# Optimization experiments

Measured on AMD Instinct MI355X. Metric: run time of the kernel, lower is better.

## Reference

```python
import jax, jax.numpy as jnp
import numpy as np

N_NODES = 100000
N_EDGES = 1600000
F_IN = 128
HID = 64
N_LAYERS = 4
N_GRAPHS = 512
N_CLASSES = 10
BN_EPS = 1e-5


def setup_inputs() -> dict:
    key = jax.random.key(0)
    ks = jax.random.split(key, 24)
    inp = {
        "x": jax.random.normal(ks[0], (N_NODES, F_IN), dtype=jnp.float32),
        "edge_index": jax.random.randint(ks[1], (2, N_EDGES), 0, N_NODES, dtype=jnp.int32),
        "batch": jnp.sort(jax.random.randint(ks[2], (N_NODES,), 0, N_GRAPHS, dtype=jnp.int32)),
        # GINConv eps (train_eps=True, init 0) per layer
        "eps": jnp.zeros((N_LAYERS,), dtype=jnp.float32),
        # layer 0 MLP (in=F_IN)
        "W1_0": jax.random.normal(ks[3], (F_IN, HID)) * 0.05,
        "b1_0": jnp.zeros((HID,)),
        "g_0": jnp.ones((HID,)),
        "be_0": jnp.zeros((HID,)),
        "W2_0": jax.random.normal(ks[4], (HID, HID)) * 0.05,
        "b2_0": jnp.zeros((HID,)),
        # layers 1..3 MLPs stacked (in=HID)
        "W1_r": jax.random.normal(ks[5], (N_LAYERS - 1, HID, HID)) * 0.05,
        "b1_r": jnp.zeros((N_LAYERS - 1, HID)),
        "g_r": jnp.ones((N_LAYERS - 1, HID)),
        "be_r": jnp.zeros((N_LAYERS - 1, HID)),
        "W2_r": jax.random.normal(ks[6], (N_LAYERS - 1, HID, HID)) * 0.05,
        "b2_r": jnp.zeros((N_LAYERS - 1, HID)),
        # head
        "lin1_W": jax.random.normal(ks[7], (N_LAYERS * HID, HID)) * 0.05,
        "lin1_b": jnp.zeros((HID,)),
        "bn_g": jnp.ones((HID,)),
        "bn_b": jnp.zeros((HID,)),
        "lin2_W": jax.random.normal(ks[8], (HID, N_CLASSES)) * 0.05,
        "lin2_b": jnp.zeros((N_CLASSES,)),
    }
    return inp


def _bn(h, g, b):
    # BatchNorm1d training-mode math: biased variance over the batch dim
    mu = h.mean(axis=0)
    var = h.var(axis=0)
    return (h - mu) * jax.lax.rsqrt(var + BN_EPS) * g + b


def _gin_conv(x, src, dst, eps, W1, b1, g, be, W2, b2):
    # sum of neighbor (source) features scattered to target nodes
    agg = jax.ops.segment_sum(x[src], dst, num_segments=N_NODES)
    h = (1.0 + eps) * x + agg
    h = jax.nn.relu(_bn(h @ W1 + b1, g, be))
    h = jax.nn.relu(h @ W2 + b2)
    return h


def reference(x, edge_index, batch, eps,
              W1_0, b1_0, g_0, be_0, W2_0, b2_0,
              W1_r, b1_r, g_r, be_r, W2_r, b2_r,
              lin1_W, lin1_b, bn_g, bn_b, lin2_W, lin2_b):
    src, dst = edge_index[0], edge_index[1]
    h = _gin_conv(x, src, dst, eps[0], W1_0, b1_0, g_0, be_0, W2_0, b2_0)
    xs = [h]
    for i in range(N_LAYERS - 1):
        h = _gin_conv(h, src, dst, eps[i + 1], W1_r[i], b1_r[i], g_r[i], be_r[i], W2_r[i], b2_r[i])
        xs.append(h)
    hcat = jnp.concatenate(xs, axis=-1)                      # [N, L*HID]
    pooled = jax.ops.segment_sum(hcat, batch, num_segments=N_GRAPHS)  # [G, L*HID]
    out = pooled @ lin1_W + lin1_b
    out = jax.nn.relu(_bn(out, bn_g, bn_b))
    # dropout: eval mode (identity)
    out = out @ lin2_W + lin2_b
    return jax.nn.log_softmax(out, axis=-1)
```

## Files before the change

### kernel.cpp

```cpp
#include <hip/hip_runtime.h>

#define N_NODES 100000
#define N_EDGES 1600000
#define F_IN 128
#define HID 64
#define NLAYERS 4
#define N_GRAPHS 512
#define N_CLASSES 10

#define NB_BUCKET 256
#define NODES_PER_BUCKET 391
#define NBLK 256
#define EDGES_PER_BLK (N_EDGES / NBLK)

#define N_TILES ((N_NODES + 63) / 64)
#define FUSED_GRID 1024
#define NAGG 2048
#define NSTAT 512

typedef unsigned int uint_t;
typedef unsigned short ushort_t;

__device__ __forceinline__ float lo_bf(uint_t w) { return __uint_as_float(w << 16); }
__device__ __forceinline__ float hi_bf(uint_t w) { return __uint_as_float(w & 0xffff0000u); }
__device__ __forceinline__ ushort_t f2bf(float f) {
    uint_t u = __float_as_uint(f);
    u += 0x7fffu + ((u >> 16) & 1u);
    return (ushort_t)(u >> 16);
}
__device__ __forceinline__ uint_t pack2(float a, float b) {
    return ((uint_t)f2bf(b) << 16) | (uint_t)f2bf(a);
}

__global__ __launch_bounds__(256) void k_zero(int* __restrict__ btotal,
                                              float* __restrict__ statsA,
                                              float* __restrict__ pooled) {
    int i = blockIdx.x * 256 + threadIdx.x;
    if (i < NB_BUCKET) btotal[i] = 0;
    if (i < NLAYERS * 128) statsA[i] = 0.f;
    if (i < N_GRAPHS * 256) pooled[i] = 0.f;
}

__global__ __launch_bounds__(512) void kb_hist(const int* __restrict__ dst,
                                               int* __restrict__ partial,
                                               int* __restrict__ btotal) {
    __shared__ int h[NB_BUCKET];
    int tid = threadIdx.x;
    if (tid < NB_BUCKET) h[tid] = 0;
    __syncthreads();
    int e0 = blockIdx.x * EDGES_PER_BLK;
    for (int i = tid; i < EDGES_PER_BLK; i += 512) {
        uint_t d = (uint_t)dst[e0 + i];
        if (d >= (uint_t)N_NODES) d = N_NODES - 1;
        atomicAdd(&h[d / NODES_PER_BUCKET], 1);
    }
    __syncthreads();
    if (tid < NB_BUCKET) {
        int c = h[tid];
        partial[blockIdx.x * NB_BUCKET + tid] = c;
        if (c) atomicAdd(&btotal[tid], c);
    }
}

__global__ __launch_bounds__(256) void kb_base(const int* __restrict__ btotal,
                                               int* __restrict__ bbase) {
    __shared__ int sh[NB_BUCKET];
    int tid = threadIdx.x;
    sh[tid] = btotal[tid];
    __syncthreads();
    for (int off = 1; off < NB_BUCKET; off <<= 1) {
        int t = (tid >= off) ? sh[tid - off] : 0;
        __syncthreads();
        sh[tid] += t;
        __syncthreads();
    }
    bbase[tid + 1] = sh[tid];
    if (tid == 0) bbase[0] = 0;
}

__global__ __launch_bounds__(256) void kb_scan(const int* __restrict__ partial,
                                               const int* __restrict__ bbase,
                                               int* __restrict__ goff) {
    __shared__ int sh[NBLK];
    int b = blockIdx.x, tid = threadIdx.x;
    sh[tid] = partial[tid * NB_BUCKET + b];
    __syncthreads();
    for (int off = 1; off < NBLK; off <<= 1) {
        int t = (tid >= off) ? sh[tid - off] : 0;
        __syncthreads();
        sh[tid] += t;
        __syncthreads();
    }
    int excl = (tid == 0) ? 0 : sh[tid - 1];
    goff[tid * NB_BUCKET + b] = bbase[b] + excl;
}

__global__ __launch_bounds__(512) void kb_scatter(const int* __restrict__ src,
                                                  const int* __restrict__ dst,
                                                  const int* __restrict__ goff,
                                                  int* __restrict__ ebuf) {
    __shared__ int cur[NB_BUCKET];
    int tid = threadIdx.x;
    if (tid < NB_BUCKET) cur[tid] = goff[blockIdx.x * NB_BUCKET + tid];
    __syncthreads();
    int e0 = blockIdx.x * EDGES_PER_BLK;
    for (int i = tid; i < EDGES_PER_BLK; i += 512) {
        uint_t d = (uint_t)dst[e0 + i];
        if (d >= (uint_t)N_NODES) d = N_NODES - 1;
        uint_t s = (uint_t)src[e0 + i];
        if (s >= (uint_t)N_NODES) s = 0;
        int b = (int)(d / NODES_PER_BUCKET);
        int dl = (int)d - b * NODES_PER_BUCKET;
        int pos = atomicAdd(&cur[b], 1);
        ebuf[pos] = (dl << 17) | (int)s;
    }
}

__global__ __launch_bounds__(512) void kb_csr(const int* __restrict__ ebuf,
                                              const int* __restrict__ bbase,
                                              int* __restrict__ row_ptr,
                                              int* __restrict__ col_src) {
    __shared__ int cnt[512];
    __shared__ int sh[512];
    __shared__ int off[512];
    int tid = threadIdx.x, b = blockIdx.x;
    int s0 = bbase[b], s1 = bbase[b + 1];
    int n = s1 - s0;
    cnt[tid] = 0;
    __syncthreads();
    for (int i = tid; i < n; i += 512) {
        int dl = ebuf[s0 + i] >> 17;
        atomicAdd(&cnt[dl], 1);
    }
    __syncthreads();
    sh[tid] = cnt[tid];
    __syncthreads();
    for (int o = 1; o < 512; o <<= 1) {
        int t = (tid >= o) ? sh[tid - o] : 0;
        __syncthreads();
        sh[tid] += t;
        __syncthreads();
    }
    off[tid] = (tid == 0) ? 0 : sh[tid - 1];
    cnt[tid] = 0;

    int node0 = b * NODES_PER_BUCKET;
    int ncnt = N_NODES - node0;
    if (ncnt > NODES_PER_BUCKET) ncnt = NODES_PER_BUCKET;
    if (tid < ncnt) row_ptr[node0 + tid] = s0 + off[tid];
    if (b == NB_BUCKET - 1 && tid == 0) row_ptr[N_NODES] = N_EDGES;
    __syncthreads();

    for (int i = tid; i < n; i += 512) {
        int v = ebuf[s0 + i];
        int dl = v >> 17;
        int r = atomicAdd(&cnt[dl], 1);
        col_src[s0 + off[dl] + r] = v & 0x1FFFF;
    }
}

__global__ __launch_bounds__(256) void k_aggregate_u(const uint2* __restrict__ y2,
                                                     const int* __restrict__ row_ptr,
                                                     const int* __restrict__ col_src,
                                                     const float* __restrict__ eps, int layer,
                                                     const float* __restrict__ b1,
                                                     uint2* __restrict__ u2) {
    int wid = threadIdx.x >> 6, lane = threadIdx.x & 63;
    int gid = lane >> 4, l4 = lane & 15;
    float one_eps = 1.0f + eps[layer];
    int stride = gridDim.x * 4;

    for (int node = blockIdx.x * 4 + wid; node < N_NODES; node += stride) {
        int e0 = row_ptr[node], e1 = row_ptr[node + 1];
        if (e0 < 0) e0 = 0;
        if (e1 > N_EDGES) e1 = N_EDGES;
        if (e1 < e0) e1 = e0;

        float4 a0 = {0.f, 0.f, 0.f, 0.f}, a1 = a0, a2 = a0, a3 = a0;

        for (int ebase = e0; ebase < e1; ebase += 64) {
            int len = e1 - ebase; if (len > 64) len = 64;
            int ci = ebase + lane; if (ci > e1 - 1) ci = e1 - 1;
            int sv = col_src[ci];
            sv = (int)min((uint_t)sv, (uint_t)(N_NODES - 1));

            int nfull = len >> 2;
            int rem = len & 3;
            int j = 0;
            for (; j + 4 <= nfull; j += 4) {
                int s0 = __shfl(sv, (j + 0) * 4 + gid, 64);
                int s1 = __shfl(sv, (j + 1) * 4 + gid, 64);
                int s2 = __shfl(sv, (j + 2) * 4 + gid, 64);
                int s3 = __shfl(sv, (j + 3) * 4 + gid, 64);
                uint2 w0 = y2[(size_t)s0 * 16 + l4];
                uint2 w1 = y2[(size_t)s1 * 16 + l4];
                uint2 w2 = y2[(size_t)s2 * 16 + l4];
                uint2 w3 = y2[(size_t)s3 * 16 + l4];
                a0.x += lo_bf(w0.x); a0.y += hi_bf(w0.x); a0.z += lo_bf(w0.y); a0.w += hi_bf(w0.y);
                a1.x += lo_bf(w1.x); a1.y += hi_bf(w1.x); a1.z += lo_bf(w1.y); a1.w += hi_bf(w1.y);
                a2.x += lo_bf(w2.x); a2.y += hi_bf(w2.x); a2.z += lo_bf(w2.y); a2.w += hi_bf(w2.y);
                a3.x += lo_bf(w3.x); a3.y += hi_bf(w3.x); a3.z += lo_bf(w3.y); a3.w += hi_bf(w3.y);
            }
            for (; j < nfull; ++j) {
                int s = __shfl(sv, j * 4 + gid, 64);
                uint2 w = y2[(size_t)s * 16 + l4];
                a0.x += lo_bf(w.x); a0.y += hi_bf(w.x); a0.z += lo_bf(w.y); a0.w += hi_bf(w.y);
            }
            if (rem) {
                int s = __shfl(sv, nfull * 4 + gid, 64);
                if (gid < rem) {
                    uint2 w = y2[(size_t)s * 16 + l4];
                    a1.x += lo_bf(w.x); a1.y += hi_bf(w.x); a1.z += lo_bf(w.y); a1.w += hi_bf(w.y);
                }
            }
        }

        float4 t;
        t.x = (a0.x + a1.x) + (a2.x + a3.x);
        t.y = (a0.y + a1.y) + (a2.y + a3.y);
        t.z = (a0.z + a1.z) + (a2.z + a3.z);
        t.w = (a0.w + a1.w) + (a2.w + a3.w);
        t.x += __shfl_xor(t.x, 16, 64); t.x += __shfl_xor(t.x, 32, 64);
        t.y += __shfl_xor(t.y, 16, 64); t.y += __shfl_xor(t.y, 32, 64);
        t.z += __shfl_xor(t.z, 16, 64); t.z += __shfl_xor(t.z, 32, 64);
        t.w += __shfl_xor(t.w, 16, 64); t.w += __shfl_xor(t.w, 32, 64);

        if (gid == 0) {
            uint2 ws = y2[(size_t)node * 16 + l4];
            float4 bb = *(const float4*)&b1[4 * l4];
            float ox = t.x + one_eps * lo_bf(ws.x) + bb.x;
            float oy = t.y + one_eps * hi_bf(ws.x) + bb.y;
            float oz = t.z + one_eps * lo_bf(ws.y) + bb.z;
            float ow = t.w + one_eps * hi_bf(ws.y) + bb.w;
            uint2 o2;
            o2.x = pack2(ox, oy);
            o2.y = pack2(oz, ow);
            u2[(size_t)node * 16 + l4] = o2;
        }
    }
}

__global__ __launch_bounds__(256) void k_stats(const uint2* __restrict__ u2,
                                               float* __restrict__ partials) {
    __shared__ float sh[256 * 8];
    int tid = threadIdx.x;
    float a[4] = {0.f, 0.f, 0.f, 0.f}, b[4] = {0.f, 0.f, 0.f, 0.f};
    for (size_t i = (size_t)blockIdx.x * 256 + tid; i < (size_t)N_NODES * 16; i += (size_t)gridDim.x * 256) {
        uint2 w = u2[i];
        float v0 = lo_bf(w.x), v1 = hi_bf(w.x), v2 = lo_bf(w.y), v3 = hi_bf(w.y);
        a[0] += v0; b[0] += v0 * v0;
        a[1] += v1; b[1] += v1 * v1;
        a[2] += v2; b[2] += v2 * v2;
        a[3] += v3; b[3] += v3 * v3;
    }
    #pragma unroll
    for (int j = 0; j < 4; ++j) { sh[tid * 8 + j] = a[j]; sh[tid * 8 + 4 + j] = b[j]; }
    __syncthreads();
    if (tid < 64) {
        int quad = tid >> 2, o = tid & 3;
        float s = 0.f, ss = 0.f;
        for (int g = 0; g < 16; ++g) {
            int t = g * 16 + quad;
            s  += sh[t * 8 + o];
            ss += sh[t * 8 + 4 + o];
        }
        partials[(size_t)blockIdx.x * 128 + tid]      = s;
        partials[(size_t)blockIdx.x * 128 + 64 + tid] = ss;
    }
}

__global__ __launch_bounds__(256) void k_redstats(const float* __restrict__ partials,
                                                  float* __restrict__ outp) {
    __shared__ float sh[256];
    int b = blockIdx.x, tid = threadIdx.x;
    float v = 0.f;
    for (int i = tid; i < NSTAT; i += 256) v += partials[(size_t)i * 128 + b];
    sh[tid] = v;
    __syncthreads();
    for (int off = 128; off > 0; off >>= 1) {
        if (tid < off) sh[tid] += sh[tid + off];
        __syncthreads();
    }
    if (tid == 0) outp[b] = sh[0];
}

template <int K>
__global__ __launch_bounds__(256) void k_gemm1(const float* __restrict__ A,
                                               const float* __restrict__ W,
                                               ushort_t* __restrict__ out) {
    constexpr int KC = 64;
    constexpr int KP = KC + 4;
    __shared__ float Al[64 * KP];
    __shared__ float Wl[KC * 64];
    int tid = threadIdx.x;
    int base = blockIdx.x * 64;
    int ct = (tid & 15) * 4;
    int rb = (tid >> 4) * 4;
    float4 acc0 = {0.f, 0.f, 0.f, 0.f}, acc1 = acc0, acc2 = acc0, acc3 = acc0;
    bool full = (base + 64 <= N_NODES);

    #pragma unroll
    for (int kc = 0; kc < K; kc += KC) {
        for (int i = tid; i < KC * 16; i += 256)
            ((float4*)Wl)[i] = ((const float4*)(W + (size_t)kc * 64))[i];
        for (int i = tid; i < 64 * (KC / 4); i += 256) {
            int row = i / (KC / 4), kq = i % (KC / 4);
            int grow = base + row;
            if (!full && grow >= N_NODES) grow = N_NODES - 1;
            float4 v = ((const float4*)(A + (size_t)grow * K + kc))[kq];
            *(float4*)&Al[row * KP + kq * 4] = v;
        }
        __syncthreads();

        const float* A0 = &Al[(rb + 0) * KP];
        const float* A1 = &Al[(rb + 1) * KP];
        const float* A2 = &Al[(rb + 2) * KP];
        const float* A3 = &Al[(rb + 3) * KP];
        #pragma unroll 4
        for (int k = 0; k < KC; ++k) {
            float4 w = *(const float4*)&Wl[k * 64 + ct];
            float a0 = A0[k], a1 = A1[k], a2 = A2[k], a3 = A3[k];
            acc0.x = fmaf(a0, w.x, acc0.x); acc0.y = fmaf(a0, w.y, acc0.y);
            acc0.z = fmaf(a0, w.z, acc0.z); acc0.w = fmaf(a0, w.w, acc0.w);
            acc1.x = fmaf(a1, w.x, acc1.x); acc1.y = fmaf(a1, w.y, acc1.y);
            acc1.z = fmaf(a1, w.z, acc1.z); acc1.w = fmaf(a1, w.w, acc1.w);
            acc2.x = fmaf(a2, w.x, acc2.x); acc2.y = fmaf(a2, w.y, acc2.y);
            acc2.z = fmaf(a2, w.z, acc2.z); acc2.w = fmaf(a2, w.w, acc2.w);
            acc3.x = fmaf(a3, w.x, acc3.x); acc3.y = fmaf(a3, w.y, acc3.y);
            acc3.z = fmaf(a3, w.z, acc3.z); acc3.w = fmaf(a3, w.w, acc3.w);
        }
        __syncthreads();
    }

    float4 accs[4] = {acc0, acc1, acc2, acc3};
    #pragma unroll
    for (int r = 0; r < 4; ++r) {
        int row = base + rb + r;
        if (row < N_NODES) {
            ushort4 o;
            o.x = f2bf(accs[r].x); o.y = f2bf(accs[r].y);
            o.z = f2bf(accs[r].z); o.w = f2bf(accs[r].w);
            *(ushort4*)&out[(size_t)row * 64 + ct] = o;
        }
    }
}

template <bool NEXT>
__global__ __launch_bounds__(256) void k_fused(const uint2* __restrict__ U2,
                                               const float* __restrict__ W2,
                                               const float* __restrict__ sums,
                                               const float* __restrict__ g_,
                                               const float* __restrict__ be,
                                               const float* __restrict__ b2,
                                               const int* __restrict__ batch,
                                               float* __restrict__ pooled, int layer,
                                               const float* __restrict__ W1n,
                                               ushort_t* __restrict__ ynext) {
    constexpr int K = 64, KP = 68;
    __shared__ float Al[64 * KP];
    __shared__ float Wl[K * 64];
    __shared__ float Pl[256];
    __shared__ __align__(16) float Sc[64];
    __shared__ __align__(16) float Sh[64];
    int tid = threadIdx.x;

    if (tid < 64) {
        const float inv_n = 1.0f / N_NODES;
        float mean = sums[tid] * inv_n;
        float var = sums[64 + tid] * inv_n - mean * mean;
        if (var < 0.f) var = 0.f;
        float inv = rsqrtf(var + 1e-5f);
        float sc = inv * g_[tid];
        Sc[tid] = sc;
        Sh[tid] = be[tid] - mean * sc;
    }
    __syncthreads();

    int ct = (tid & 15) * 4;
    int rb = (tid >> 4) * 4;
    int r0 = tid >> 4, q0 = tid & 15;
    float4 scv = *(const float4*)&Sc[q0 * 4];
    float4 shv = *(const float4*)&Sh[q0 * 4];

    uint2 up0, up1, up2, up3;

    {
        int base = blockIdx.x * 64;
        int g0 = base + r0, g1 = base + r0 + 16, g2 = base + r0 + 32, g3 = base + r0 + 48;
        if (g0 > N_NODES - 1) g0 = N_NODES - 1;
        if (g1 > N_NODES - 1) g1 = N_NODES - 1;
        if (g2 > N_NODES - 1) g2 = N_NODES - 1;
        if (g3 > N_NODES - 1) g3 = N_NODES - 1;
        up0 = U2[(size_t)g0 * 16 + q0];
        up1 = U2[(size_t)g1 * 16 + q0];
        up2 = U2[(size_t)g2 * 16 + q0];
        up3 = U2[(size_t)g3 * 16 + q0];
    }

    for (int tile = blockIdx.x; tile < N_TILES; tile += gridDim.x) {
        int base = tile * 64;

        for (int i = tid; i < K * 16; i += 256)
            ((float4*)Wl)[i] = ((const float4*)W2)[i];
        {
            #define UNPK(UR, RR) { \
                float4 v = {lo_bf((UR).x), hi_bf((UR).x), lo_bf((UR).y), hi_bf((UR).y)}; \
                v.x = fmaxf(fmaf(v.x, scv.x, shv.x), 0.f); \
                v.y = fmaxf(fmaf(v.y, scv.y, shv.y), 0.f); \
                v.z = fmaxf(fmaf(v.z, scv.z, shv.z), 0.f); \
                v.w = fmaxf(fmaf(v.w, scv.w, shv.w), 0.f); \
                *(float4*)&Al[(RR) * KP + q0 * 4] = v; }
            UNPK(up0, r0);
            UNPK(up1, r0 + 16);
            UNPK(up2, r0 + 32);
            UNPK(up3, r0 + 48);
            #undef UNPK
        }
        __syncthreads();

        float4 acc0 = {0.f, 0.f, 0.f, 0.f}, acc1 = acc0, acc2 = acc0, acc3 = acc0;
        {
            const float* A0 = &Al[(rb + 0) * KP];
            const float* A1 = &Al[(rb + 1) * KP];
            const float* A2 = &Al[(rb + 2) * KP];
            const float* A3 = &Al[(rb + 3) * KP];
            #pragma unroll 4
            for (int k = 0; k < K; ++k) {
                float4 w = *(const float4*)&Wl[k * 64 + ct];
                float a0 = A0[k], a1 = A1[k], a2 = A2[k], a3 = A3[k];
                acc0.x = fmaf(a0, w.x, acc0.x); acc0.y = fmaf(a0, w.y, acc0.y);
                acc0.z = fmaf(a0, w.z, acc0.z); acc0.w = fmaf(a0, w.w, acc0.w);
                acc1.x = fmaf(a1, w.x, acc1.x); acc1.y = fmaf(a1, w.y, acc1.y);
                acc1.z = fmaf(a1, w.z, acc1.z); acc1.w = fmaf(a1, w.w, acc1.w);
                acc2.x = fmaf(a2, w.x, acc2.x); acc2.y = fmaf(a2, w.y, acc2.y);
                acc2.z = fmaf(a2, w.z, acc2.z); acc2.w = fmaf(a2, w.w, acc2.w);
                acc3.x = fmaf(a3, w.x, acc3.x); acc3.y = fmaf(a3, w.y, acc3.y);
                acc3.z = fmaf(a3, w.z, acc3.z); acc3.w = fmaf(a3, w.w, acc3.w);
            }
        }
        __syncthreads();

        {
            float4 bb = *(const float4*)&b2[ct];
            float4 accs[4] = {acc0, acc1, acc2, acc3};
            #pragma unroll
            for (int r = 0; r < 4; ++r) {
                float4 o;
                o.x = fmaxf(accs[r].x + bb.x, 0.f);
                o.y = fmaxf(accs[r].y + bb.y, 0.f);
                o.z = fmaxf(accs[r].z + bb.z, 0.f);
                o.w = fmaxf(accs[r].w + bb.w, 0.f);
                *(float4*)&Al[(rb + r) * KP + ct] = o;
            }
        }
        if (NEXT) {
            for (int i = tid; i < K * 16; i += 256)
                ((float4*)Wl)[i] = ((const float4*)W1n)[i];
        }
        __syncthreads();

        if (NEXT) {
            float4 y0 = {0.f, 0.f, 0.f, 0.f}, y1 = y0, y2_ = y0, y3 = y0;
            const float* A0 = &Al[(rb + 0) * KP];
            const float* A1 = &Al[(rb + 1) * KP];
            const float* A2 = &Al[(rb + 2) * KP];
            const float* A3 = &Al[(rb + 3) * KP];
            #pragma unroll 4
            for (int k = 0; k < K; ++k) {
                float4 w = *(const float4*)&Wl[k * 64 + ct];
                float a0 = A0[k], a1 = A1[k], a2 = A2[k], a3 = A3[k];
                y0.x = fmaf(a0, w.x, y0.x); y0.y = fmaf(a0, w.y, y0.y);
                y0.z = fmaf(a0, w.z, y0.z); y0.w = fmaf(a0, w.w, y0.w);
                y1.x = fmaf(a1, w.x, y1.x); y1.y = fmaf(a1, w.y, y1.y);
                y1.z = fmaf(a1, w.z, y1.z); y1.w = fmaf(a1, w.w, y1.w);
                y2_.x = fmaf(a2, w.x, y2_.x); y2_.y = fmaf(a2, w.y, y2_.y);
                y2_.z = fmaf(a2, w.z, y2_.z); y2_.w = fmaf(a2, w.w, y2_.w);
                y3.x = fmaf(a3, w.x, y3.x); y3.y = fmaf(a3, w.y, y3.y);
                y3.z = fmaf(a3, w.z, y3.z); y3.w = fmaf(a3, w.w, y3.w);
            }
            float4 ys[4] = {y0, y1, y2_, y3};
            #pragma unroll
            for (int r = 0; r < 4; ++r) {
                int row = base + rb + r;
                if (row < N_NODES) {
                    ushort4 o;
                    o.x = f2bf(ys[r].x); o.y = f2bf(ys[r].y);
                    o.z = f2bf(ys[r].z); o.w = f2bf(ys[r].w);
                    *(ushort4*)&ynext[(size_t)row * 64 + ct] = o;
                }
            }
        }

        {
            int nt = tile + gridDim.x;
            if (nt < N_TILES) {
                int nb = nt * 64;
                int g0 = nb + r0, g1 = nb + r0 + 16, g2 = nb + r0 + 32, g3 = nb + r0 + 48;
                if (g0 > N_NODES - 1) g0 = N_NODES - 1;
                if (g1 > N_NODES - 1) g1 = N_NODES - 1;
                if (g2 > N_NODES - 1) g2 = N_NODES - 1;
                if (g3 > N_NODES - 1) g3 = N_NODES - 1;
                up0 = U2[(size_t)g0 * 16 + q0];
                up1 = U2[(size_t)g1 * 16 + q0];
                up2 = U2[(size_t)g2 * 16 + q0];
                up3 = U2[(size_t)g3 * 16 + q0];
            }
        }

        {
            int lastEx = base + 64; if (lastEx > N_NODES) lastEx = N_NODES;
            int gstart = batch[base];
            int gend = batch[lastEx - 1];
            if (gstart < 0) gstart = 0;
            if (gend > N_GRAPHS - 1) gend = N_GRAPHS - 1;
            int col = tid & 63, q = tid >> 6;
            int rs = base;
            for (int g = gstart; g <= gend; ++g) {
                int lo = rs, hi = lastEx;
                while (lo < hi) { int mid = (lo + hi) >> 1; if (batch[mid] <= g) lo = mid + 1; else hi = mid; }
                int re = lo;
                float s = 0.f;
                for (int r = rs + q; r < re; r += 4) s += Al[(r - base) * KP + col];
                Pl[tid] = s;
                __syncthreads();
                if (tid < 64) {
                    float tot = (Pl[col] + Pl[64 + col]) + (Pl[128 + col] + Pl[192 + col]);
                    atomicAdd(&pooled[g * 256 + layer * 64 + col], tot);
                }
                __syncthreads();
                rs = re;
            }
        }
        __syncthreads();
    }
}

__global__ __launch_bounds__(64) void k_head1(const float* __restrict__ pooled,
                                              const float* __restrict__ W, const float* __restrict__ b,
                                              float* __restrict__ t1) {
    __shared__ __align__(16) float pl[256];
    int g = blockIdx.x, lane = threadIdx.x;
    ((float4*)pl)[lane] = ((const float4*)(pooled + g * 256))[lane];
    __syncthreads();
    float acc = b[lane];
    for (int k = 0; k < 256; ++k) acc += pl[k] * W[k * 64 + lane];
    t1[g * 64 + lane] = acc;
}

__global__ __launch_bounds__(64) void k_head3(const float* __restrict__ t1,
                                              const float* __restrict__ g_, const float* __restrict__ b_,
                                              const float* __restrict__ W2, const float* __restrict__ b2,
                                              float* __restrict__ out) {
    __shared__ float v[64];
    __shared__ float o[16];
    int g = blockIdx.x, lane = threadIdx.x;
    float s = 0.f, q = 0.f;
    for (int r = 0; r < N_GRAPHS; ++r) {
        float vv = t1[r * 64 + lane];
        s += vv; q += vv * vv;
    }
    float mean = s * (1.0f / N_GRAPHS);
    float var = q * (1.0f / N_GRAPHS) - mean * mean;
    if (var < 0.f) var = 0.f;
    float inv = rsqrtf(var + 1e-5f);
    float sc = inv * g_[lane];
    float sh = b_[lane] - mean * sc;
    float x = t1[g * 64 + lane] * sc + sh;
    v[lane] = fmaxf(x, 0.f);
    __syncthreads();
    if (lane < N_CLASSES) {
        float acc = b2[lane];
        for (int k = 0; k < 64; ++k) acc += v[k] * W2[k * N_CLASSES + lane];
        o[lane] = acc;
    }
    __syncthreads();
    if (lane < N_CLASSES) {
        float m = -1e30f;
        for (int k = 0; k < N_CLASSES; ++k) m = fmaxf(m, o[k]);
        float ssum = 0.f;
        for (int k = 0; k < N_CLASSES; ++k) ssum += expf(o[k] - m);
        out[g * N_CLASSES + lane] = o[lane] - m - logf(ssum);
    }
}

extern "C" void kernel_launch(void* const* d_in, const int* in_sizes, int n_in,
                              void* d_out, int out_size, void* d_ws, size_t ws_size,
                              hipStream_t stream) {
    const float* x      = (const float*)d_in[0];
    const int*   ei     = (const int*)d_in[1];
    const int*   srcArr = ei;
    const int*   dstArr = ei + N_EDGES;
    const int*   batch  = (const int*)d_in[2];
    const float* eps    = (const float*)d_in[3];
    const float* W1_0   = (const float*)d_in[4];
    const float* b1_0   = (const float*)d_in[5];
    const float* g_0    = (const float*)d_in[6];
    const float* be_0   = (const float*)d_in[7];
    const float* W2_0   = (const float*)d_in[8];
    const float* b2_0   = (const float*)d_in[9];
    const float* W1_r   = (const float*)d_in[10];
    const float* b1_r   = (const float*)d_in[11];
    const float* g_r    = (const float*)d_in[12];
    const float* be_r   = (const float*)d_in[13];
    const float* W2_r   = (const float*)d_in[14];
    const float* b2_r   = (const float*)d_in[15];
    const float* lin1W  = (const float*)d_in[16];
    const float* lin1b  = (const float*)d_in[17];
    const float* bn_g   = (const float*)d_in[18];
    const float* bn_b   = (const float*)d_in[19];
    const float* lin2W  = (const float*)d_in[20];
    const float* lin2b  = (const float*)d_in[21];

    char* ws = (char*)d_ws;
    auto alloc = [&](size_t bytes) {
        char* p = ws;
        ws += (bytes + 255) & ~(size_t)255;
        return p;
    };
    int*      row_ptr = (int*)alloc(((size_t)N_NODES + 1) * 4);
    int*      col_src = (int*)alloc((size_t)N_EDGES * 4);
    int*      ebuf    = (int*)alloc((size_t)N_EDGES * 4);
    int*      partial = (int*)alloc((size_t)NBLK * NB_BUCKET * 4);
    int*      goff    = (int*)alloc((size_t)NBLK * NB_BUCKET * 4);
    int*      btotal  = (int*)alloc((size_t)NB_BUCKET * 4);
    int*      bbase   = (int*)alloc(((size_t)NB_BUCKET + 1) * 4);
    ushort_t* ybf     = (ushort_t*)alloc((size_t)N_NODES * 64 * 2);
    ushort_t* ubf     = (ushort_t*)alloc((size_t)N_NODES * 64 * 2);
    float*    statsA  = (float*)alloc(NLAYERS * 128 * 4);
    float*    pooled  = (float*)alloc((size_t)N_GRAPHS * 256 * 4);
    float*    t1      = (float*)alloc((size_t)N_GRAPHS * 64 * 4);
    float*    spart   = (float*)ebuf;

    k_zero<<<(N_GRAPHS * 256 + 255) / 256, 256, 0, stream>>>(btotal, statsA, pooled);
    kb_hist<<<NBLK, 512, 0, stream>>>(dstArr, partial, btotal);
    kb_base<<<1, 256, 0, stream>>>(btotal, bbase);
    kb_scan<<<NB_BUCKET, 256, 0, stream>>>(partial, bbase, goff);
    kb_scatter<<<NBLK, 512, 0, stream>>>(srcArr, dstArr, goff, ebuf);
    kb_csr<<<NB_BUCKET, 512, 0, stream>>>(ebuf, bbase, row_ptr, col_src);

    const int gemm_grid = (N_NODES + 63) / 64;

    k_gemm1<128><<<gemm_grid, 256, 0, stream>>>(x, W1_0, ybf);

    for (int l = 0; l < NLAYERS; ++l) {
        const float *b1, *gg, *be, *W2, *b2;
        if (l == 0) { b1 = b1_0; gg = g_0; be = be_0; W2 = W2_0; b2 = b2_0; }
        else {
            b1 = b1_r + (size_t)(l - 1) * 64;
            gg = g_r  + (size_t)(l - 1) * 64;
            be = be_r + (size_t)(l - 1) * 64;
            W2 = W2_r + (size_t)(l - 1) * 64 * 64;
            b2 = b2_r + (size_t)(l - 1) * 64;
        }
        k_aggregate_u<<<NAGG, 256, 0, stream>>>((const uint2*)ybf, row_ptr, col_src, eps, l, b1,
                                                (uint2*)ubf);
        k_stats<<<NSTAT, 256, 0, stream>>>((const uint2*)ubf, spart);
        k_redstats<<<128, 256, 0, stream>>>(spart, statsA + l * 128);
        if (l < NLAYERS - 1) {
            const float* W1n = W1_r + (size_t)l * 64 * 64;
            k_fused<true><<<FUSED_GRID, 256, 0, stream>>>((const uint2*)ubf, W2, statsA + l * 128, gg, be, b2,
                                                          batch, pooled, l, W1n, ybf);
        } else {
            k_fused<false><<<FUSED_GRID, 256, 0, stream>>>((const uint2*)ubf, W2, statsA + l * 128, gg, be, b2,
                                                           batch, pooled, l, nullptr, nullptr);
        }
    }

    k_head1<<<N_GRAPHS, 64, 0, stream>>>(pooled, lin1W, lin1b, t1);
    k_head3<<<N_GRAPHS, 64, 0, stream>>>(t1, bn_g, bn_b, lin2W, lin2b, (float*)d_out);
}
```

Before: 521.1 us.

## Prefetch next node's edge list in aggregation and drop small scan/reduce kernels

The aggregation kernel now loads the next node's row_ptr range and first 64 source indices ahead of processing the current node, hiding the dependent index-load latency behind the current gather. The separate bucket-base scan kernel is folded into kb_scan and kb_csr, which each recompute the prefix sum locally. The stats partial-reduction kernel is replaced by float atomicAdd into the per-layer sums. Together these remove several launches and a serial latency chain, at the cost of redundant scans per block and nondeterministic float summation order.

```diff
diff --git a/kernel.cpp b/kernel.cpp
--- a/kernel.cpp
+++ b/kernel.cpp
@@ -62,27 +62,24 @@
     }
 }
 
-__global__ __launch_bounds__(256) void kb_base(const int* __restrict__ btotal,
-                                               int* __restrict__ bbase) {
-    __shared__ int sh[NB_BUCKET];
-    int tid = threadIdx.x;
-    sh[tid] = btotal[tid];
-    __syncthreads();
-    for (int off = 1; off < NB_BUCKET; off <<= 1) {
-        int t = (tid >= off) ? sh[tid - off] : 0;
-        __syncthreads();
-        sh[tid] += t;
-        __syncthreads();
-    }
-    bbase[tid + 1] = sh[tid];
-    if (tid == 0) bbase[0] = 0;
-}
 
 __global__ __launch_bounds__(256) void kb_scan(const int* __restrict__ partial,
-                                               const int* __restrict__ bbase,
+                                               const int* __restrict__ btotal,
                                                int* __restrict__ goff) {
     __shared__ int sh[NBLK];
     int b = blockIdx.x, tid = threadIdx.x;
+
+    sh[tid] = btotal[tid];
+    __syncthreads();
+    for (int off = 1; off < NB_BUCKET; off <<= 1) {
+        int t = (tid >= off) ? sh[tid - off] : 0;
+        __syncthreads();
+        sh[tid] += t;
+        __syncthreads();
+    }
+    int bb = (b == 0) ? 0 : sh[b - 1];
+    __syncthreads();
+
     sh[tid] = partial[tid * NB_BUCKET + b];
     __syncthreads();
     for (int off = 1; off < NBLK; off <<= 1) {
@@ -92,7 +89,7 @@
         __syncthreads();
     }
     int excl = (tid == 0) ? 0 : sh[tid - 1];
-    goff[tid * NB_BUCKET + b] = bbase[b] + excl;
+    goff[tid * NB_BUCKET + b] = bb + excl;
 }
 
 __global__ __launch_bounds__(512) void kb_scatter(const int* __restrict__ src,
@@ -117,15 +114,28 @@
 }
 
 __global__ __launch_bounds__(512) void kb_csr(const int* __restrict__ ebuf,
-                                              const int* __restrict__ bbase,
+                                              const int* __restrict__ btotal,
                                               int* __restrict__ row_ptr,
                                               int* __restrict__ col_src) {
     __shared__ int cnt[512];
     __shared__ int sh[512];
     __shared__ int off[512];
+    __shared__ int shb[NB_BUCKET];
     int tid = threadIdx.x, b = blockIdx.x;
-    int s0 = bbase[b], s1 = bbase[b + 1];
+
+    if (tid < NB_BUCKET) shb[tid] = btotal[tid];
+    __syncthreads();
+    for (int o = 1; o < NB_BUCKET; o <<= 1) {
+        int t = 0;
+        if (tid < NB_BUCKET && tid >= o) t = shb[tid - o];
+        __syncthreads();
+        if (tid < NB_BUCKET) shb[tid] += t;
+        __syncthreads();
+    }
+    int s0 = (b == 0) ? 0 : shb[b - 1];
+    int s1 = shb[b];
     int n = s1 - s0;
+
     cnt[tid] = 0;
     __syncthreads();
     for (int i = tid; i < n; i += 512) {
@@ -158,6 +168,38 @@
         col_src[s0 + off[dl] + r] = v & 0x1FFFF;
     }
 }
+
+#define GIN_BATCH(SVv, LENv)                                                        \
+    {                                                                               \
+        int nfull_ = (LENv) >> 2, rem_ = (LENv) & 3;                                \
+        int j_ = 0;                                                                 \
+        for (; j_ + 4 <= nfull_; j_ += 4) {                                         \
+            int s0_ = __shfl((SVv), (j_ + 0) * 4 + gid, 64);                        \
+            int s1_ = __shfl((SVv), (j_ + 1) * 4 + gid, 64);                        \
+            int s2_ = __shfl((SVv), (j_ + 2) * 4 + gid, 64);                        \
+            int s3_ = __shfl((SVv), (j_ + 3) * 4 + gid, 64);                        \
+            uint2 w0_ = y2[(size_t)s0_ * 16 + l4];                                  \
+            uint2 w1_ = y2[(size_t)s1_ * 16 + l4];                                  \
+            uint2 w2_ = y2[(size_t)s2_ * 16 + l4];                                  \
+            uint2 w3_ = y2[(size_t)s3_ * 16 + l4];                                  \
+            a0.x += lo_bf(w0_.x); a0.y += hi_bf(w0_.x); a0.z += lo_bf(w0_.y); a0.w += hi_bf(w0_.y); \
+            a1.x += lo_bf(w1_.x); a1.y += hi_bf(w1_.x); a1.z += lo_bf(w1_.y); a1.w += hi_bf(w1_.y); \
+            a2.x += lo_bf(w2_.x); a2.y += hi_bf(w2_.x); a2.z += lo_bf(w2_.y); a2.w += hi_bf(w2_.y); \
+            a3.x += lo_bf(w3_.x); a3.y += hi_bf(w3_.x); a3.z += lo_bf(w3_.y); a3.w += hi_bf(w3_.y); \
+        }                                                                           \
+        for (; j_ < nfull_; ++j_) {                                                 \
+            int s_ = __shfl((SVv), j_ * 4 + gid, 64);                               \
+            uint2 w_ = y2[(size_t)s_ * 16 + l4];                                    \
+            a0.x += lo_bf(w_.x); a0.y += hi_bf(w_.x); a0.z += lo_bf(w_.y); a0.w += hi_bf(w_.y); \
+        }                                                                           \
+        if (rem_) {                                                                 \
+            int s_ = __shfl((SVv), nfull_ * 4 + gid, 64);                           \
+            if (gid < rem_) {                                                       \
+                uint2 w_ = y2[(size_t)s_ * 16 + l4];                                \
+                a1.x += lo_bf(w_.x); a1.y += hi_bf(w_.x); a1.z += lo_bf(w_.y); a1.w += hi_bf(w_.y); \
+            }                                                                       \
+        }                                                                           \
+    }
 
 __global__ __launch_bounds__(256) void k_aggregate_u(const uint2* __restrict__ y2,
                                                      const int* __restrict__ row_ptr,
@@ -170,49 +212,50 @@
     float one_eps = 1.0f + eps[layer];
     int stride = gridDim.x * 4;
 
-    for (int node = blockIdx.x * 4 + wid; node < N_NODES; node += stride) {
-        int e0 = row_ptr[node], e1 = row_ptr[node + 1];
-        if (e0 < 0) e0 = 0;
-        if (e1 > N_EDGES) e1 = N_EDGES;
-        if (e1 < e0) e1 = e0;
+    int node = blockIdx.x * 4 + wid;
+    if (node >= N_NODES) return;
+
+    int e0 = row_ptr[node], e1 = row_ptr[node + 1];
+    if (e0 < 0) e0 = 0;
+    if (e1 > N_EDGES) e1 = N_EDGES;
+    if (e1 < e0) e1 = e0;
+    int ci = e0 + lane;
+    if (ci > e1 - 1) ci = e1 - 1;
+    if (ci < 0) ci = 0;
+    int sv = col_src[ci];
+    sv = (int)min((uint_t)sv, (uint_t)(N_NODES - 1));
+
+    for (; node < N_NODES; node += stride) {
+        int nxt = node + stride;
+        int ne0 = 0, ne1 = 0;
+        if (nxt < N_NODES) {
+            ne0 = row_ptr[nxt];
+            ne1 = row_ptr[nxt + 1];
+        }
+        if (ne0 < 0) ne0 = 0;
+        if (ne1 > N_EDGES) ne1 = N_EDGES;
+        if (ne1 < ne0) ne1 = ne0;
 
         float4 a0 = {0.f, 0.f, 0.f, 0.f}, a1 = a0, a2 = a0, a3 = a0;
 
-        for (int ebase = e0; ebase < e1; ebase += 64) {
-            int len = e1 - ebase; if (len > 64) len = 64;
-            int ci = ebase + lane; if (ci > e1 - 1) ci = e1 - 1;
-            int sv = col_src[ci];
-            sv = (int)min((uint_t)sv, (uint_t)(N_NODES - 1));
-
-            int nfull = len >> 2;
-            int rem = len & 3;
-            int j = 0;
-            for (; j + 4 <= nfull; j += 4) {
-                int s0 = __shfl(sv, (j + 0) * 4 + gid, 64);
-                int s1 = __shfl(sv, (j + 1) * 4 + gid, 64);
-                int s2 = __shfl(sv, (j + 2) * 4 + gid, 64);
-                int s3 = __shfl(sv, (j + 3) * 4 + gid, 64);
-                uint2 w0 = y2[(size_t)s0 * 16 + l4];
-                uint2 w1 = y2[(size_t)s1 * 16 + l4];
-                uint2 w2 = y2[(size_t)s2 * 16 + l4];
-                uint2 w3 = y2[(size_t)s3 * 16 + l4];
-                a0.x += lo_bf(w0.x); a0.y += hi_bf(w0.x); a0.z += lo_bf(w0.y); a0.w += hi_bf(w0.y);
-                a1.x += lo_bf(w1.x); a1.y += hi_bf(w1.x); a1.z += lo_bf(w1.y); a1.w += hi_bf(w1.y);
-                a2.x += lo_bf(w2.x); a2.y += hi_bf(w2.x); a2.z += lo_bf(w2.y); a2.w += hi_bf(w2.y);
-                a3.x += lo_bf(w3.x); a3.y += hi_bf(w3.x); a3.z += lo_bf(w3.y); a3.w += hi_bf(w3.y);
-            }
-            for (; j < nfull; ++j) {
-                int s = __shfl(sv, j * 4 + gid, 64);
-                uint2 w = y2[(size_t)s * 16 + l4];
-                a0.x += lo_bf(w.x); a0.y += hi_bf(w.x); a0.z += lo_bf(w.y); a0.w += hi_bf(w.y);
-            }
-            if (rem) {
-                int s = __shfl(sv, nfull * 4 + gid, 64);
-                if (gid < rem) {
-                    uint2 w = y2[(size_t)s * 16 + l4];
-                    a1.x += lo_bf(w.x); a1.y += hi_bf(w.x); a1.z += lo_bf(w.y); a1.w += hi_bf(w.y);
-                }
-            }
+        int lenb = e1 - e0;
+        if (lenb > 64) lenb = 64;
+        GIN_BATCH(sv, lenb);
+
+        int nci = ne0 + lane;
+        if (nci > ne1 - 1) nci = ne1 - 1;
+        if (nci < 0) nci = 0;
+        int nsv = col_src[nci];
+        nsv = (int)min((uint_t)nsv, (uint_t)(N_NODES - 1));
+
+        for (int ebase = e0 + 64; ebase < e1; ebase += 64) {
+            int len2 = e1 - ebase;
+            if (len2 > 64) len2 = 64;
+            int ci2 = ebase + lane;
+            if (ci2 > e1 - 1) ci2 = e1 - 1;
+            int sv2 = col_src[ci2];
+            sv2 = (int)min((uint_t)sv2, (uint_t)(N_NODES - 1));
+            GIN_BATCH(sv2, len2);
         }
 
         float4 t;
@@ -237,11 +280,12 @@
             o2.y = pack2(oz, ow);
             u2[(size_t)node * 16 + l4] = o2;
         }
-    }
-}
-
-__global__ __launch_bounds__(256) void k_stats(const uint2* __restrict__ u2,
-                                               float* __restrict__ partials) {
+
+        e0 = ne0; e1 = ne1; sv = nsv;
+    }
+}
+
+__global__ __launch_bounds__(256) void k_stats(const uint2* __restrict__ u2, float* __restrict__ sums) {
     __shared__ float sh[256 * 8];
     int tid = threadIdx.x;
     float a[4] = {0.f, 0.f, 0.f, 0.f}, b[4] = {0.f, 0.f, 0.f, 0.f};
@@ -264,24 +308,9 @@
             s  += sh[t * 8 + o];
             ss += sh[t * 8 + 4 + o];
         }
-        partials[(size_t)blockIdx.x * 128 + tid]      = s;
-        partials[(size_t)blockIdx.x * 128 + 64 + tid] = ss;
-    }
-}
-
-__global__ __launch_bounds__(256) void k_redstats(const float* __restrict__ partials,
-                                                  float* __restrict__ outp) {
-    __shared__ float sh[256];
-    int b = blockIdx.x, tid = threadIdx.x;
-    float v = 0.f;
-    for (int i = tid; i < NSTAT; i += 256) v += partials[(size_t)i * 128 + b];
-    sh[tid] = v;
-    __syncthreads();
-    for (int off = 128; off > 0; off >>= 1) {
-        if (tid < off) sh[tid] += sh[tid + off];
-        __syncthreads();
-    }
-    if (tid == 0) outp[b] = sh[0];
+        atomicAdd(&sums[tid], s);
+        atomicAdd(&sums[64 + tid], ss);
+    }
 }
 
 template <int K>
@@ -623,20 +652,17 @@
     int*      partial = (int*)alloc((size_t)NBLK * NB_BUCKET * 4);
     int*      goff    = (int*)alloc((size_t)NBLK * NB_BUCKET * 4);
     int*      btotal  = (int*)alloc((size_t)NB_BUCKET * 4);
-    int*      bbase   = (int*)alloc(((size_t)NB_BUCKET + 1) * 4);
     ushort_t* ybf     = (ushort_t*)alloc((size_t)N_NODES * 64 * 2);
     ushort_t* ubf     = (ushort_t*)alloc((size_t)N_NODES * 64 * 2);
     float*    statsA  = (float*)alloc(NLAYERS * 128 * 4);
     float*    pooled  = (float*)alloc((size_t)N_GRAPHS * 256 * 4);
     float*    t1      = (float*)alloc((size_t)N_GRAPHS * 64 * 4);
-    float*    spart   = (float*)ebuf;
 
     k_zero<<<(N_GRAPHS * 256 + 255) / 256, 256, 0, stream>>>(btotal, statsA, pooled);
     kb_hist<<<NBLK, 512, 0, stream>>>(dstArr, partial, btotal);
-    kb_base<<<1, 256, 0, stream>>>(btotal, bbase);
-    kb_scan<<<NB_BUCKET, 256, 0, stream>>>(partial, bbase, goff);
+    kb_scan<<<NB_BUCKET, 256, 0, stream>>>(partial, btotal, goff);
     kb_scatter<<<NBLK, 512, 0, stream>>>(srcArr, dstArr, goff, ebuf);
-    kb_csr<<<NB_BUCKET, 512, 0, stream>>>(ebuf, bbase, row_ptr, col_src);
+    kb_csr<<<NB_BUCKET, 512, 0, stream>>>(ebuf, btotal, row_ptr, col_src);
 
     const int gemm_grid = (N_NODES + 63) / 64;
 
@@ -654,8 +680,7 @@
         }
         k_aggregate_u<<<NAGG, 256, 0, stream>>>((const uint2*)ybf, row_ptr, col_src, eps, l, b1,
                                                 (uint2*)ubf);
-        k_stats<<<NSTAT, 256, 0, stream>>>((const uint2*)ubf, spart);
-        k_redstats<<<128, 256, 0, stream>>>(spart, statsA + l * 128);
+        k_stats<<<NSTAT, 256, 0, stream>>>((const uint2*)ubf, statsA + l * 128);
         if (l < NLAYERS - 1) {
             const float* W1n = W1_r + (size_t)l * 64 * 64;
             k_fused<true><<<FUSED_GRID, 256, 0, stream>>>((const uint2*)ubf, W2, statsA + l * 128, gg, be, b2,
```

After: 551.4 us. 5.8% more time.
